# Performance work log

Hardware: AMD Instinct MI355X
Metric: run time of the kernel (lower is better)

The kernel has to match this reference:

```python
import jax, jax.numpy as jnp
import numpy as np

B, C, T = 16, 256, 2048
K = 1024  # codes per layer
N_LAYERS = 3


def setup_inputs() -> dict:
    key = jax.random.key(0)
    kx, k0, k1, k2 = jax.random.split(key, 4)
    x = jax.random.normal(kx, (B, C, T), dtype=jnp.float32)
    scale = 1.0 / K
    emb0 = jax.random.uniform(k0, (K, C), minval=-scale, maxval=scale, dtype=jnp.float32)
    emb1 = jax.random.uniform(k1, (K, C), minval=-scale, maxval=scale, dtype=jnp.float32)
    emb2 = jax.random.uniform(k2, (K, C), minval=-scale, maxval=scale, dtype=jnp.float32)
    return {"x": x, "emb0": emb0, "emb1": emb1, "emb2": emb2}


def _vq_layer(x, emb):
    # x: [B, C, T], emb: [K, C]
    b, c, t = x.shape
    flat = jnp.transpose(x, (0, 2, 1)).reshape(-1, c)          # [B*T, C]
    # squared L2 distance to each code: ||f||^2 - 2 f.e + ||e||^2
    dist = (jnp.sum(flat * flat, axis=1, keepdims=True)
            - 2.0 * flat @ emb.T
            + jnp.sum(emb * emb, axis=1))                       # [B*T, K]
    idx = jnp.argmin(dist, axis=1)                              # [B*T]
    quant = jnp.transpose(emb[idx].reshape(b, t, c), (0, 2, 1)) # [B, C, T]
    sg = jax.lax.stop_gradient
    loss = jnp.mean((sg(quant) - x) ** 2) + jnp.mean((quant - sg(x)) ** 2)
    quantized = x + sg(quant - x)  # straight-through
    return quantized, loss


def reference(x, emb0, emb1, emb2):
    total_loss = jnp.float32(0.0)
    out = x
    for emb in (emb0, emb1, emb2):
        out, loss = _vq_layer(out, emb)
        total_loss = total_loss + loss
    return out, total_loss
```

## Files before the change

### kernel.cpp

```cpp
#include <hip/hip_runtime.h>
#include <stdint.h>

#define B_  16
#define C_  256
#define T_  2048
#define K_  1024
#define TOTAL_ELEMS 8388608

typedef short bf16x8 __attribute__((ext_vector_type(8)));
typedef float f32x4 __attribute__((ext_vector_type(4)));

__device__ __forceinline__ unsigned long long pack_key(float d, int idx) {
  unsigned u = __float_as_uint(d);
  u = (u & 0x80000000u) ? ~u : (u | 0x80000000u);
  return ((unsigned long long)u << 32) | (unsigned)idx;
}
__device__ __forceinline__ float unpack_dist(unsigned long long key) {
  unsigned du = (unsigned)(key >> 32);
  unsigned bits = (du & 0x80000000u) ? (du ^ 0x80000000u) : ~du;
  return __uint_as_float(bits);
}

__device__ __forceinline__ unsigned short f2bf_rne(float f) {
  unsigned u = __float_as_uint(f);
  unsigned r = u + 0x7FFFu + ((u >> 16) & 1u);
  return (unsigned short)(r >> 16);
}

__device__ __forceinline__ void gload_lds16(const void* g, void* l) {
  __builtin_amdgcn_global_load_lds(
      (const __attribute__((address_space(1))) unsigned int*)g,
      (__attribute__((address_space(3))) unsigned int*)l, 16, 0, 0);
}

__global__ __launch_bounds__(256) void prep_kernel(
    const float* __restrict__ e0, const float* __restrict__ e1,
    const float* __restrict__ e2, float* __restrict__ nrm,
    unsigned short* __restrict__ ebf, uint4* __restrict__ keys_region,
    float* __restrict__ loss_accum) {
  int bid = blockIdx.x;
  int tid = threadIdx.x;
  if (bid < 12) {
    int i = bid * 256 + tid;
    const float* e = (i < 1024) ? e0 : (i < 2048) ? e1 : e2;
    const float* p = e + (size_t)(i & 1023) * C_;
    float s = 0.0f;
    for (int c = 0; c < C_; c += 4) {
      float4 v = *(const float4*)(p + c);
      s = fmaf(v.x, v.x, s); s = fmaf(v.y, v.y, s);
      s = fmaf(v.z, v.z, s); s = fmaf(v.w, v.w, s);
    }
    nrm[i] = s;
  } else if (bid < 268) {
    int i = (bid - 12) * 256 + tid;
    float4 v = *(const float4*)(e0 + (size_t)i * 4);
    unsigned lo = (unsigned)f2bf_rne(v.x) | ((unsigned)f2bf_rne(v.y) << 16);
    unsigned hi = (unsigned)f2bf_rne(v.z) | ((unsigned)f2bf_rne(v.w) << 16);
    *(uint2*)(ebf + (size_t)i * 4) = make_uint2(lo, hi);
  } else {
    int i = (bid - 268) * 256 + tid;
    keys_region[i] = make_uint4(0xFFFFFFFFu, 0xFFFFFFFFu, 0xFFFFFFFFu, 0xFFFFFFFFu);
    if (bid == 268 && tid == 0) *loss_accum = 0.0f;
  }
}

__global__ __launch_bounds__(256) void xpose_kernel(
    const float* __restrict__ x, unsigned short* __restrict__ xT,
    float* __restrict__ loss_accum) {
  __shared__ float ftile[64][68];
  __shared__ float red[4];
  int tid = threadIdx.x;
  int bid = blockIdx.x;
  int b  = bid >> 7;
  int t0 = ((bid >> 2) & 31) << 6;
  int c0 = (bid & 3) << 6;
  int cr = tid >> 4;
  int t_loc = (tid & 15) * 4;
  const float* src = x + (size_t)b * (C_ * T_) + (size_t)c0 * T_ + t0;
  float sq = 0.0f;
#pragma unroll
  for (int q = 0; q < 4; q++) {
    int c_loc = cr + q * 16;
    float4 v = *(const float4*)(src + (size_t)c_loc * T_ + t_loc);
    *(float4*)&ftile[c_loc][t_loc] = v;
    sq = fmaf(v.x, v.x, sq); sq = fmaf(v.y, v.y, sq);
    sq = fmaf(v.z, v.z, sq); sq = fmaf(v.w, v.w, sq);
  }
  for (int off = 32; off > 0; off >>= 1) sq += __shfl_down(sq, off, 64);
  if ((tid & 63) == 0) red[tid >> 6] = sq;
  __syncthreads();
  if (tid == 0)
    atomicAdd(loss_accum, red[0] + red[1] + red[2] + red[3]);

  int t_row = tid >> 2;
  int cs = (tid & 3) * 16;
  unsigned pk[8];
#pragma unroll
  for (int i = 0; i < 8; i++) {
    unsigned short lo = f2bf_rne(ftile[cs + 2 * i][t_row]);
    unsigned short hi = f2bf_rne(ftile[cs + 2 * i + 1][t_row]);
    pk[i] = (unsigned)lo | ((unsigned)hi << 16);
  }
  unsigned short* dst = xT + ((size_t)(b * T_ + t0 + t_row) * C_ + c0 + cs);
  *(uint4*)dst       = make_uint4(pk[0], pk[1], pk[2], pk[3]);
  *((uint4*)dst + 1) = make_uint4(pk[4], pk[5], pk[6], pk[7]);
}

__global__ __launch_bounds__(256) void map_tile_kernel(
    const float* __restrict__ e0, const float* __restrict__ e1,
    const float* __restrict__ e2, const float* __restrict__ nrm,
    unsigned long long* __restrict__ keysM) {
  __shared__ float As[16][68];
  __shared__ float Bs[16][68];
  int bid = blockIdx.x;
  int m = bid >> 8;
  int tb = bid & 255;
  int ar0 = (tb >> 4) << 6;
  int br0 = (tb & 15) << 6;
  const float* Ap = m ? e1 : e0;
  const float* Bp = m ? e2 : e1;
  const float* nB = nrm + (m + 1) * 1024;

  int tid = threadIdx.x;
  int ty = tid >> 4, tx = tid & 15;
  int srow = tid >> 2;
  int skp  = (tid & 3) << 2;

  float acc[4][4];
#pragma unroll
  for (int i = 0; i < 4; i++)
#pragma unroll
    for (int j = 0; j < 4; j++) acc[i][j] = 0.0f;

  const float* gA = Ap + (size_t)(ar0 + srow) * C_ + skp;
  const float* gB = Bp + (size_t)(br0 + srow) * C_ + skp;

  for (int kk = 0; kk < C_; kk += 16) {
    float4 av = *(const float4*)(gA + kk);
    float4 bv = *(const float4*)(gB + kk);
    __syncthreads();
    As[skp + 0][srow] = av.x; As[skp + 1][srow] = av.y;
    As[skp + 2][srow] = av.z; As[skp + 3][srow] = av.w;
    Bs[skp + 0][srow] = bv.x; Bs[skp + 1][srow] = bv.y;
    Bs[skp + 2][srow] = bv.z; Bs[skp + 3][srow] = bv.w;
    __syncthreads();
#pragma unroll
    for (int k = 0; k < 16; k++) {
      float4 a4 = *(const float4*)&As[k][ty * 4];
      float4 b4 = *(const float4*)&Bs[k][tx * 4];
      float aa[4] = {a4.x, a4.y, a4.z, a4.w};
      float bb[4] = {b4.x, b4.y, b4.z, b4.w};
#pragma unroll
      for (int i = 0; i < 4; i++)
#pragma unroll
        for (int j = 0; j < 4; j++)
          acc[i][j] = fmaf(aa[i], bb[j], acc[i][j]);
    }
  }

  float nv[4];
#pragma unroll
  for (int j = 0; j < 4; j++) nv[j] = nB[br0 + tx * 4 + j];

#pragma unroll
  for (int i = 0; i < 4; i++) {
    unsigned long long best = 0xFFFFFFFFFFFFFFFFULL;
#pragma unroll
    for (int j = 0; j < 4; j++) {
      int code = br0 + tx * 4 + j;
      float s = nv[j] - 2.0f * acc[i][j];
      unsigned long long key = pack_key(s, code);
      if (key < best) best = key;
    }
#pragma unroll
    for (int off = 1; off < 16; off <<= 1) {
      unsigned long long o = __shfl_xor(best, off, 64);
      if (o < best) best = o;
    }
    if (tx == 0)
      atomicMin(&keysM[m * 1024 + ar0 + ty * 4 + i], best);
  }
}

__global__ __launch_bounds__(256) void l0_mfma_kernel(
    const unsigned short* __restrict__ xT, const unsigned short* __restrict__ ebf,
    const float* __restrict__ e0n, unsigned long long* __restrict__ keys) {
  __shared__ __align__(16) unsigned short AB[2][2][128][32];
  __shared__ unsigned long long kred[128][2];

  int tid = threadIdx.x;
  int l = tid & 63, w = tid >> 6;
  int wr = w >> 1, wc = w & 1;
  int mb = blockIdx.x & 255, nb = blockIdx.x >> 8;
  int row0 = mb << 7, kb = nb << 7;

  int sm = w * 32 + (l >> 2);
  int ks = (l & 3) ^ ((l >> 3) & 3);
  const unsigned short* gA = xT + ((size_t)(row0 + sm) * C_ + ks * 8);
  const unsigned short* gB = ebf + ((size_t)(kb + sm) * C_ + ks * 8);

  f32x4 acc[4][4];
#pragma unroll
  for (int mi = 0; mi < 4; mi++)
#pragma unroll
    for (int ni = 0; ni < 4; ni++) acc[mi][ni] = (f32x4){0.f, 0.f, 0.f, 0.f};

#define STAGE(buf, kk) do {                                              \
    char* baseA = (char*)&AB[(buf)][0][0][0] + w * 2048;                 \
    char* baseB = (char*)&AB[(buf)][1][0][0] + w * 2048;                 \
    gload_lds16(gA + (size_t)(kk) * 32, baseA);                          \
    gload_lds16(gA + (size_t)16 * C_ + (size_t)(kk) * 32, baseA + 1024); \
    gload_lds16(gB + (size_t)(kk) * 32, baseB);                          \
    gload_lds16(gB + (size_t)16 * C_ + (size_t)(kk) * 32, baseB + 1024); \
  } while (0)

  STAGE(0, 0);
  __syncthreads();

  int lr = l & 15, lg = l >> 4;
  int slot = lg ^ ((lr >> 1) & 3);
  int buf = 0;
  for (int kk = 0; kk < 8; kk++) {
    if (kk < 7) STAGE(buf ^ 1, kk + 1);
    bf16x8 aF[4], bF[4];
#pragma unroll
    for (int mi = 0; mi < 4; mi++)
      aF[mi] = *(const bf16x8*)&AB[buf][0][wr * 64 + mi * 16 + lr][slot * 8];
#pragma unroll
    for (int ni = 0; ni < 4; ni++)
      bF[ni] = *(const bf16x8*)&AB[buf][1][wc * 64 + ni * 16 + lr][slot * 8];
#pragma unroll
    for (int mi = 0; mi < 4; mi++)
#pragma unroll
      for (int ni = 0; ni < 4; ni++)
        acc[mi][ni] = __builtin_amdgcn_mfma_f32_16x16x32_bf16(
            aF[mi], bF[ni], acc[mi][ni], 0, 0, 0);
    __syncthreads();
    buf ^= 1;
  }
#undef STAGE

  float nv[4];
#pragma unroll
  for (int ni = 0; ni < 4; ni++) nv[ni] = e0n[kb + wc * 64 + ni * 16 + lr];

#pragma unroll
  for (int mi = 0; mi < 4; mi++) {
#pragma unroll
    for (int r = 0; r < 4; r++) {
      unsigned long long best = 0xFFFFFFFFFFFFFFFFULL;
#pragma unroll
      for (int ni = 0; ni < 4; ni++) {
        int code = kb + wc * 64 + ni * 16 + lr;
        float s = nv[ni] - 2.0f * acc[mi][ni][r];
        unsigned long long key = pack_key(s, code);
        if (key < best) best = key;
      }
#pragma unroll
      for (int off = 1; off < 16; off <<= 1) {
        unsigned long long o = __shfl_xor(best, off, 64);
        if (o < best) best = o;
      }
      if (lr == 0) kred[wr * 64 + mi * 16 + lg * 4 + r][wc] = best;
    }
  }
  __syncthreads();
  if (tid < 128) {
    unsigned long long b0 = kred[tid][0], b1 = kred[tid][1];
    atomicMin(&keys[row0 + tid], b0 < b1 ? b0 : b1);
  }
}

__global__ __launch_bounds__(256) void finish_kernel(
    const float* __restrict__ emb2,
    const unsigned long long* __restrict__ keys,
    const unsigned long long* __restrict__ keysM,
    const float* __restrict__ nrm,
    float* __restrict__ out, float* __restrict__ loss_accum) {
  __shared__ int code2_l[64];
  __shared__ float rloss[64];
  int tid = threadIdx.x;
  int b  = blockIdx.x >> 5;
  int t0 = (blockIdx.x & 31) << 6;
  int tt = tid & 63, w = tid >> 6;

  if (w == 0) {
    unsigned long long key0 = keys[(size_t)b * T_ + t0 + tt];
    int idx0 = (int)(key0 & 0xFFFFFFFFULL);
    float s0 = unpack_dist(key0);
    unsigned long long k1 = keysM[idx0];
    int c1 = (int)(k1 & 0xFFFFFFFFULL);
    unsigned long long k2 = keysM[1024 + c1];
    code2_l[tt] = (int)(k2 & 0xFFFFFFFFULL);
    rloss[tt] = s0 + nrm[idx0] + unpack_dist(k1) + nrm[1024 + c1] + unpack_dist(k2);
  }
  __syncthreads();

  float* ob = out + ((size_t)b << 19);
  int code2 = code2_l[tt];
  const float* e2row = emb2 + (size_t)code2 * C_;
  for (int c4 = w * 64; c4 < w * 64 + 64; c4 += 4) {
    float4 ev = *(const float4*)(e2row + c4);
    float evv[4] = {ev.x, ev.y, ev.z, ev.w};
#pragma unroll
    for (int u = 0; u < 4; u++)
      ob[(size_t)(c4 + u) * T_ + t0 + tt] = evv[u];
  }
  if (w == 0) {
    float tot = rloss[tt];
    for (int off = 32; off > 0; off >>= 1)
      tot += __shfl_down(tot, off, 64);
    if (tt == 0) atomicAdd(loss_accum, tot);
  }
}

__global__ void finalize_kernel(const float* __restrict__ loss_accum,
                                float* __restrict__ out_loss) {
  *out_loss = 2.0f * (*loss_accum) / 8388608.0f;
}

extern "C" void kernel_launch(void* const* d_in, const int* in_sizes, int n_in,
                              void* d_out, int out_size, void* d_ws, size_t ws_size,
                              hipStream_t stream) {
  const float* x  = (const float*)d_in[0];
  const float* e0 = (const float*)d_in[1];
  const float* e1 = (const float*)d_in[2];
  const float* e2 = (const float*)d_in[3];
  float* out = (float*)d_out;
  char* ws = (char*)d_ws;

  unsigned long long* keys  = (unsigned long long*)ws;
  unsigned long long* keysM = (unsigned long long*)(ws + 262144);
  float* nrm  = (float*)(ws + 278528);
  float* loss_accum = (float*)(ws + 290816);
  unsigned short* embbf = (unsigned short*)(ws + 294912);
  unsigned short* xT    = (unsigned short*)(ws + 819200);

  prep_kernel<<<336, 256, 0, stream>>>(e0, e1, e2, nrm, embbf, (uint4*)ws, loss_accum);
  xpose_kernel<<<2048, 256, 0, stream>>>(x, xT, loss_accum);
  l0_mfma_kernel<<<2048, 256, 0, stream>>>(xT, embbf, nrm, keys);
  map_tile_kernel<<<512, 256, 0, stream>>>(e0, e1, e2, nrm, keysM);
  finish_kernel<<<512, 256, 0, stream>>>(e2, keys, keysM, nrm, out, loss_accum);
  finalize_kernel<<<1, 1, 0, stream>>>(loss_accum, out + TOTAL_ELEMS);
}
```

Measured before the change: 115.4 us.

## Make L0 MFMA blocks own row tiles and sweep all codes with register argmin

Each block of the layer-0 distance kernel now keeps its 128 bf16 rows resident in 64KB of dynamic LDS. It streams all 1024 codebook rows through a double-buffered B tile and tracks the running argmax in registers, with accumulators pre-seeded by -0.5*||e||^2. This drops the repeated A loads across code blocks, removes the 64-bit atomicMin merges and the keys-buffer initialisation, and shrinks the prep grid. In exchange the grid falls from 2048 to 256 blocks with one 4-wave block per CU, so latency hiding is weaker. The longer in-block pipeline could also leave the kernel stalled on memory.

```diff
diff --git a/kernel.cpp b/kernel.cpp
--- a/kernel.cpp
+++ b/kernel.cpp
@@ -36,7 +36,7 @@
 __global__ __launch_bounds__(256) void prep_kernel(
     const float* __restrict__ e0, const float* __restrict__ e1,
     const float* __restrict__ e2, float* __restrict__ nrm,
-    unsigned short* __restrict__ ebf, uint4* __restrict__ keys_region,
+    unsigned short* __restrict__ ebf, uint4* __restrict__ keysM_region,
     float* __restrict__ loss_accum) {
   int bid = blockIdx.x;
   int tid = threadIdx.x;
@@ -59,7 +59,7 @@
     *(uint2*)(ebf + (size_t)i * 4) = make_uint2(lo, hi);
   } else {
     int i = (bid - 268) * 256 + tid;
-    keys_region[i] = make_uint4(0xFFFFFFFFu, 0xFFFFFFFFu, 0xFFFFFFFFu, 0xFFFFFFFFu);
+    keysM_region[i] = make_uint4(0xFFFFFFFFu, 0xFFFFFFFFu, 0xFFFFFFFFu, 0xFFFFFFFFu);
     if (bid == 268 && tid == 0) *loss_accum = 0.0f;
   }
 }
@@ -182,92 +182,127 @@
   }
 }
 
-__global__ __launch_bounds__(256) void l0_mfma_kernel(
+__global__ __launch_bounds__(256, 1) void l0_mfma_kernel(
     const unsigned short* __restrict__ xT, const unsigned short* __restrict__ ebf,
     const float* __restrict__ e0n, unsigned long long* __restrict__ keys) {
-  __shared__ __align__(16) unsigned short AB[2][2][128][32];
-  __shared__ unsigned long long kred[128][2];
+  extern __shared__ char smem[];
+  char* Abuf = smem;
+  char* Bbuf = smem + 65536;
 
   int tid = threadIdx.x;
   int l = tid & 63, w = tid >> 6;
   int wr = w >> 1, wc = w & 1;
-  int mb = blockIdx.x & 255, nb = blockIdx.x >> 8;
-  int row0 = mb << 7, kb = nb << 7;
-
-  int sm = w * 32 + (l >> 2);
-  int ks = (l & 3) ^ ((l >> 3) & 3);
-  const unsigned short* gA = xT + ((size_t)(row0 + sm) * C_ + ks * 8);
-  const unsigned short* gB = ebf + ((size_t)(kb + sm) * C_ + ks * 8);
-
-  f32x4 acc[4][4];
+  int row0 = blockIdx.x << 7;
+  int lr = l & 15, lg = l >> 4;
+
+  {
+    char* abase = Abuf + w * 16384;
+    int q = (l & 31) >> 2;
+    int s = l & 3;
+    int rsub = l >> 5;
+#pragma unroll
+    for (int i = 0; i < 16; i++) {
+      int row = w * 32 + i * 2 + rsub;
+      int kelem = (((q ^ ((row >> 2) & 1)) << 5) + ((s ^ (row & 3)) << 3));
+      gload_lds16(xT + (((size_t)(row0 + row)) << 8) + kelem, abase + i * 1024);
+    }
+  }
+
+#define STAGEB(d, p, kk) do {                                            \
+    char* bbase = Bbuf + (d) * 16384 + w * 4096;                         \
+    _Pragma("unroll")                                                    \
+    for (int i_ = 0; i_ < 4; i_++) {                                     \
+      int code_ = (p) * 256 + w * 64 + i_ * 16 + (l >> 2);               \
+      int kelem_ = ((kk) << 5) + (((l & 3) ^ (code_ & 3)) << 3);         \
+      gload_lds16(ebf + (((size_t)code_) << 8) + kelem_, bbase + i_ * 1024); \
+    } } while (0)
+
+  f32x4 acc[2][4][4];
+  float bestv[4][4];
+  int   bestm[4][4];
 #pragma unroll
   for (int mi = 0; mi < 4; mi++)
 #pragma unroll
-    for (int ni = 0; ni < 4; ni++) acc[mi][ni] = (f32x4){0.f, 0.f, 0.f, 0.f};
-
-#define STAGE(buf, kk) do {                                              \
-    char* baseA = (char*)&AB[(buf)][0][0][0] + w * 2048;                 \
-    char* baseB = (char*)&AB[(buf)][1][0][0] + w * 2048;                 \
-    gload_lds16(gA + (size_t)(kk) * 32, baseA);                          \
-    gload_lds16(gA + (size_t)16 * C_ + (size_t)(kk) * 32, baseA + 1024); \
-    gload_lds16(gB + (size_t)(kk) * 32, baseB);                          \
-    gload_lds16(gB + (size_t)16 * C_ + (size_t)(kk) * 32, baseB + 1024); \
-  } while (0)
-
-  STAGE(0, 0);
+    for (int r = 0; r < 4; r++) { bestv[mi][r] = -1e30f; bestm[mi][r] = 0; }
+
+  STAGEB(0, 0, 0);
   __syncthreads();
 
-  int lr = l & 15, lg = l >> 4;
-  int slot = lg ^ ((lr >> 1) & 3);
-  int buf = 0;
-  for (int kk = 0; kk < 8; kk++) {
-    if (kk < 7) STAGE(buf ^ 1, kk + 1);
-    bf16x8 aF[4], bF[4];
+  int aseg = (lg ^ (lr & 3)) << 4;
+  int akb1 = (lr >> 2) & 1;
+  int d = 0;
+  for (int p = 0; p < 4; p++) {
+#pragma unroll
+    for (int c01 = 0; c01 < 2; c01++)
+#pragma unroll
+      for (int ni = 0; ni < 4; ni++) {
+        float iv = -0.5f * e0n[p * 256 + c01 * 128 + wc * 64 + ni * 16 + lr];
+        f32x4 ivv = {iv, iv, iv, iv};
+#pragma unroll
+        for (int mi = 0; mi < 4; mi++) acc[c01][mi][ni] = ivv;
+      }
+#pragma unroll
+    for (int kk = 0; kk < 8; kk++) {
+      if (kk < 7) { STAGEB(d ^ 1, p, kk + 1); }
+      else if (p < 3) { STAGEB(d ^ 1, p + 1, 0); }
+      bf16x8 aF[4], bF[2][4];
+#pragma unroll
+      for (int mi = 0; mi < 4; mi++)
+        aF[mi] = *(const bf16x8*)(Abuf + (wr * 64 + mi * 16 + lr) * 512 +
+                                  ((kk ^ akb1) << 6) + aseg);
+#pragma unroll
+      for (int c01 = 0; c01 < 2; c01++)
+#pragma unroll
+        for (int ni = 0; ni < 4; ni++)
+          bF[c01][ni] = *(const bf16x8*)(Bbuf + d * 16384 +
+                        (c01 * 128 + wc * 64 + ni * 16 + lr) * 64 + aseg);
+#pragma unroll
+      for (int c01 = 0; c01 < 2; c01++)
+#pragma unroll
+        for (int mi = 0; mi < 4; mi++)
+#pragma unroll
+          for (int ni = 0; ni < 4; ni++)
+            acc[c01][mi][ni] = __builtin_amdgcn_mfma_f32_16x16x32_bf16(
+                aF[mi], bF[c01][ni], acc[c01][mi][ni], 0, 0, 0);
+      __syncthreads();
+      d ^= 1;
+    }
+    int pm = p * 8;
 #pragma unroll
     for (int mi = 0; mi < 4; mi++)
-      aF[mi] = *(const bf16x8*)&AB[buf][0][wr * 64 + mi * 16 + lr][slot * 8];
-#pragma unroll
-    for (int ni = 0; ni < 4; ni++)
-      bF[ni] = *(const bf16x8*)&AB[buf][1][wc * 64 + ni * 16 + lr][slot * 8];
-#pragma unroll
-    for (int mi = 0; mi < 4; mi++)
-#pragma unroll
-      for (int ni = 0; ni < 4; ni++)
-        acc[mi][ni] = __builtin_amdgcn_mfma_f32_16x16x32_bf16(
-            aF[mi], bF[ni], acc[mi][ni], 0, 0, 0);
-    __syncthreads();
-    buf ^= 1;
-  }
-#undef STAGE
-
-  float nv[4];
-#pragma unroll
-  for (int ni = 0; ni < 4; ni++) nv[ni] = e0n[kb + wc * 64 + ni * 16 + lr];
-
-#pragma unroll
-  for (int mi = 0; mi < 4; mi++) {
+#pragma unroll
+      for (int r = 0; r < 4; r++)
+#pragma unroll
+        for (int c01 = 0; c01 < 2; c01++)
+#pragma unroll
+          for (int ni = 0; ni < 4; ni++) {
+            float v = acc[c01][mi][ni][r];
+            if (v > bestv[mi][r]) { bestv[mi][r] = v; bestm[mi][r] = pm + c01 * 4 + ni; }
+          }
+  }
+#undef STAGEB
+
+  unsigned long long (*kred)[2] = (unsigned long long(*)[2])Bbuf;
+#pragma unroll
+  for (int mi = 0; mi < 4; mi++)
 #pragma unroll
     for (int r = 0; r < 4; r++) {
-      unsigned long long best = 0xFFFFFFFFFFFFFFFFULL;
-#pragma unroll
-      for (int ni = 0; ni < 4; ni++) {
-        int code = kb + wc * 64 + ni * 16 + lr;
-        float s = nv[ni] - 2.0f * acc[mi][ni][r];
-        unsigned long long key = pack_key(s, code);
-        if (key < best) best = key;
+      float sdist = -2.0f * bestv[mi][r];
+      int m = bestm[mi][r];
+      int code = ((m >> 3) << 8) | (((m >> 2) & 1) << 7) | (wc << 6) |
+                 ((m & 3) << 4) | lr;
+      unsigned long long key = pack_key(sdist, code);
+#pragma unroll
+      for (int off = 1; off < 16; off <<= 1) {
+        unsigned long long o = __shfl_xor(key, off, 64);
+        if (o < key) key = o;
       }
-#pragma unroll
-      for (int off = 1; off < 16; off <<= 1) {
-        unsigned long long o = __shfl_xor(best, off, 64);
-        if (o < best) best = o;
-      }
-      if (lr == 0) kred[wr * 64 + mi * 16 + lg * 4 + r][wc] = best;
-    }
-  }
+      if (lr == 0) kred[wr * 64 + mi * 16 + lg * 4 + r][wc] = key;
+    }
   __syncthreads();
   if (tid < 128) {
-    unsigned long long b0 = kred[tid][0], b1 = kred[tid][1];
-    atomicMin(&keys[row0 + tid], b0 < b1 ? b0 : b1);
+    unsigned long long a = kred[tid][0], b = kred[tid][1];
+    keys[row0 + tid] = a < b ? a : b;
   }
 }
 
@@ -336,9 +371,9 @@
   unsigned short* embbf = (unsigned short*)(ws + 294912);
   unsigned short* xT    = (unsigned short*)(ws + 819200);
 
-  prep_kernel<<<336, 256, 0, stream>>>(e0, e1, e2, nrm, embbf, (uint4*)ws, loss_accum);
+  prep_kernel<<<272, 256, 0, stream>>>(e0, e1, e2, nrm, embbf, (uint4*)keysM, loss_accum);
   xpose_kernel<<<2048, 256, 0, stream>>>(x, xT, loss_accum);
-  l0_mfma_kernel<<<2048, 256, 0, stream>>>(xT, embbf, nrm, keys);
+  l0_mfma_kernel<<<256, 256, 98304, stream>>>(xT, embbf, nrm, keys);
   map_tile_kernel<<<512, 256, 0, stream>>>(e0, e1, e2, nrm, keysM);
   finish_kernel<<<512, 256, 0, stream>>>(e2, keys, keysM, nrm, out, loss_accum);
   finalize_kernel<<<1, 1, 0, stream>>>(loss_accum, out + TOTAL_ELEMS);
```

Result: faster. 110.7 us (-4.1%).
